# Performance work log

Hardware: AMD Instinct MI355X
Metric: run time of the kernel (lower is better)

The kernel has to match this reference:

```python
import jax, jax.numpy as jnp
import numpy as np

N_NODES = 100000
N_EDGES = 3200000
N_FEAT = 16
N_GRAPHS = 1024


def setup_inputs() -> dict:
    key = jax.random.key(0)
    ks = jax.random.split(key, 12)
    x = jax.random.normal(ks[0], (N_NODES, N_FEAT), dtype=jnp.float32)
    edge_index = jax.random.randint(ks[1], (2, N_EDGES), 0, N_NODES, dtype=jnp.int32)
    batch = jnp.sort(jax.random.randint(ks[2], (N_NODES,), 0, N_GRAPHS, dtype=jnp.int32))
    def lin(k, fan_in, fan_out):
        s = 1.0 / np.sqrt(fan_in)
        return jax.random.uniform(k, (fan_in, fan_out), jnp.float32, -s, s)
    W1 = lin(ks[3], N_FEAT, 64); b1 = jnp.zeros((64,), jnp.float32)
    W2 = lin(ks[4], 64, 32);     b2 = jnp.zeros((32,), jnp.float32)
    fc1_W = lin(ks[5], 32, 16);  fc1_b = jnp.zeros((16,), jnp.float32)
    fc2_W = lin(ks[6], 16, 1);   fc2_b = jnp.zeros((1,), jnp.float32)
    return {"x": x, "edge_index": edge_index, "batch": batch,
            "W1": W1, "b1": b1, "W2": W2, "b2": b2,
            "fc1_W": fc1_W, "fc1_b": fc1_b, "fc2_W": fc2_W, "fc2_b": fc2_b}


def _gcn_conv(h, W, b, src, dst, norm, n_nodes):
    # h: [N, Fin] -> [N, Fout]; symmetric-normalized scatter-add (PyG GCNConv)
    h = h @ W
    msg = h[src] * norm[:, None]            # edge-wise gather + scale
    out = jax.ops.segment_sum(msg, dst, num_segments=n_nodes)
    return out + b


def reference(x, edge_index, batch, W1, b1, W2, b2, fc1_W, fc1_b, fc2_W, fc2_b):
    n_nodes = x.shape[0]
    # add self-loops
    loops = jnp.arange(n_nodes, dtype=edge_index.dtype)
    src = jnp.concatenate([edge_index[0], loops])
    dst = jnp.concatenate([edge_index[1], loops])
    deg = jax.ops.segment_sum(jnp.ones_like(dst, dtype=x.dtype), dst, num_segments=n_nodes)
    dinv = jnp.where(deg > 0, jax.lax.rsqrt(deg), 0.0)
    norm = dinv[src] * dinv[dst]

    h = jax.nn.relu(_gcn_conv(x, W1, b1, src, dst, norm, n_nodes))
    # dropout p=0.2 is identity at inference
    h = jax.nn.relu(_gcn_conv(h, W2, b2, src, dst, norm, n_nodes))

    # global mean pool over graphs
    sums = jax.ops.segment_sum(h, batch, num_segments=N_GRAPHS)
    cnts = jax.ops.segment_sum(jnp.ones((n_nodes,), h.dtype), batch, num_segments=N_GRAPHS)
    g = sums / jnp.maximum(cnts, 1.0)[:, None]

    g = jax.nn.relu(g @ fc1_W + fc1_b)
    # dropout p=0.5 is identity at inference
    out = g @ fc2_W + fc2_b
    return jax.nn.sigmoid(out)  # [N_GRAPHS, 1]
```

## Files before the change

kernel.cpp:

```cpp
#include <hip/hip_runtime.h>
#include <math.h>

#define NNODES  100000
#define NEDGES  3200000
#define NGRAPHS 1024
#define BNODES  196
#define NBUCK   ((NNODES + BNODES - 1) / BNODES)
#define SCAP    12288
#define SLDS    7168
#define CHUNK   4096
#define NCHUNKS ((NEDGES + CHUNK - 1) / CHUNK)

typedef int iv4 __attribute__((ext_vector_type(4)));
typedef float fv2 __attribute__((ext_vector_type(2)));

#if defined(__has_builtin)
#if __has_builtin(__builtin_amdgcn_cvt_pk_f32_fp8) && __has_builtin(__builtin_amdgcn_cvt_pk_fp8_f32)
#define HW_FP8 1
#endif
#endif

__device__ __forceinline__ unsigned bf16pair(float a, float b) {
    unsigned ua = __float_as_uint(a), ub = __float_as_uint(b);
    ua += 0x7fffu + ((ua >> 16) & 1u);
    ub += 0x7fffu + ((ub >> 16) & 1u);
    return (ua >> 16) | (ub & 0xffff0000u);
}
__device__ __forceinline__ float bflo(unsigned u) { return __uint_as_float(u << 16); }
__device__ __forceinline__ float bfhi(unsigned u) { return __uint_as_float(u & 0xffff0000u); }

__device__ __forceinline__ unsigned fp8_of(float v) {
    unsigned s = (__float_as_uint(v) >> 24) & 0x80u;
    float a = fminf(fabsf(v), 448.f);
    unsigned ub = __float_as_uint(a);
    unsigned lsb = (ub >> 20) & 1u;
    ub += 0x0007FFFFu + lsb;
    int em = (int)(ub >> 20) - (120 << 3);
    if (em < 1) return s;
    if (em > 0x7E) em = 0x7E;
    return s | (unsigned)em;
}
__device__ __forceinline__ float fp8_to_f(unsigned b) {
    unsigned em = b & 0x7Fu;
    unsigned s = (b & 0x80u) << 24;
    float f = __uint_as_float(s | ((em + 0x3C0u) << 20));
    return (em >= 8u) ? f : 0.f;
}
__device__ __forceinline__ unsigned fp8x4_pack(float a, float b, float c, float d) {
    a = fminf(fmaxf(a, -448.f), 448.f);
    b = fminf(fmaxf(b, -448.f), 448.f);
    c = fminf(fmaxf(c, -448.f), 448.f);
    d = fminf(fmaxf(d, -448.f), 448.f);
#ifdef HW_FP8
    int w = __builtin_amdgcn_cvt_pk_fp8_f32(a, b, 0, false);
    w = __builtin_amdgcn_cvt_pk_fp8_f32(c, d, w, true);
    return (unsigned)w;
#else
    return fp8_of(a) | (fp8_of(b) << 8) | (fp8_of(c) << 16) | (fp8_of(d) << 24);
#endif
}
__device__ __forceinline__ fv2 f8lo(unsigned w) {
#ifdef HW_FP8
    return __builtin_amdgcn_cvt_pk_f32_fp8((int)w, false);
#else
    fv2 t; t.x = fp8_to_f(w & 0xFFu); t.y = fp8_to_f((w >> 8) & 0xFFu); return t;
#endif
}
__device__ __forceinline__ fv2 f8hi(unsigned w) {
#ifdef HW_FP8
    return __builtin_amdgcn_cvt_pk_f32_fp8((int)w, true);
#else
    fv2 t; t.x = fp8_to_f((w >> 16) & 0xFFu); t.y = fp8_to_f(w >> 24); return t;
#endif
}


__global__ void zero4_kernel(int4* p, int nvec) {
    int i = blockIdx.x * blockDim.x + threadIdx.x;
    if (i < nvec) p[i] = make_int4(0, 0, 0, 0);
}


__global__ void binA_kernel(const int* __restrict__ src, const int* __restrict__ dst,
                            int* __restrict__ bucketCur, int* __restrict__ stage) {
    __shared__ int lcnt[NBUCK + 1];
    __shared__ int boff[NBUCK + 1];
    __shared__ int gbase[NBUCK + 1];
    __shared__ int cur[NBUCK + 1];
    __shared__ int wtot[4];
    __shared__ int packed[CHUNK];
    __shared__ unsigned short bof[CHUNK];
    int tid = threadIdx.x;
    int beg = blockIdx.x * CHUNK;
    int end = beg + CHUNK; if (end > NEDGES) end = NEDGES;
    int cnt = end - beg;

    for (int i = tid; i <= NBUCK; i += 256) lcnt[i] = 0;
    __syncthreads();

    int ent[16];
    int bk[16];
#pragma unroll
    for (int it = 0; it < 4; ++it) {
        int e0 = beg + tid * 4 + it * 1024;
        if (e0 < end) {
            iv4 d4 = __builtin_nontemporal_load((const iv4*)(dst + e0));
            iv4 s4 = __builtin_nontemporal_load((const iv4*)(src + e0));
            int b;
            b = d4.x / BNODES; ent[it*4+0] = s4.x | ((d4.x - b*BNODES) << 17); bk[it*4+0] = b; atomicAdd(&lcnt[b], 1);
            b = d4.y / BNODES; ent[it*4+1] = s4.y | ((d4.y - b*BNODES) << 17); bk[it*4+1] = b; atomicAdd(&lcnt[b], 1);
            b = d4.z / BNODES; ent[it*4+2] = s4.z | ((d4.z - b*BNODES) << 17); bk[it*4+2] = b; atomicAdd(&lcnt[b], 1);
            b = d4.w / BNODES; ent[it*4+3] = s4.w | ((d4.w - b*BNODES) << 17); bk[it*4+3] = b; atomicAdd(&lcnt[b], 1);
        } else {
            bk[it*4+0] = -1; bk[it*4+1] = -1; bk[it*4+2] = -1; bk[it*4+3] = -1;
            ent[it*4+0] = 0; ent[it*4+1] = 0; ent[it*4+2] = 0; ent[it*4+3] = 0;
        }
    }
    __syncthreads();

    int b0 = 2 * tid, b1 = 2 * tid + 1;
    int c0 = lcnt[b0];
    int c1 = (b1 < NBUCK) ? lcnt[b1] : 0;
    int sum = c0 + c1;
    int lane = tid & 63, wid = tid >> 6;
    int v = sum;
#pragma unroll
    for (int o = 1; o < 64; o <<= 1) {
        int t = __shfl_up(v, o, 64);
        if (lane >= o) v += t;
    }
    if (lane == 63) wtot[wid] = v;
    __syncthreads();
    int woff = 0;
#pragma unroll
    for (int w = 0; w < 4; ++w) woff += (w < wid) ? wtot[w] : 0;
    int excl = woff + v - sum;
    boff[b0] = excl; cur[b0] = excl;
    if (b1 < NBUCK) { boff[b1] = excl + c0; cur[b1] = excl + c0; }
    if (c0 > 0) gbase[b0] = atomicAdd(&bucketCur[b0], c0);
    if (b1 < NBUCK && c1 > 0) gbase[b1] = atomicAdd(&bucketCur[b1], c1);
    __syncthreads();

#pragma unroll
    for (int k = 0; k < 16; ++k) {
        int b = bk[k];
        if (b >= 0) {
            int p = atomicAdd(&cur[b], 1);
            packed[p] = ent[k];
            bof[p] = (unsigned short)b;
        }
    }
    __syncthreads();

    for (int i = tid; i < cnt; i += 256) {
        int b = bof[i];
        int addr = b * SCAP + gbase[b] + (i - boff[b]);
        stage[addr] = packed[i];
    }
}


__global__ void scanE_kernel(const int* __restrict__ bucketCur, int* __restrict__ ebase) {
    int lane = threadIdx.x;
    int run = 0;
    for (int base = 0; base < NBUCK; base += 64) {
        int idx = base + lane;
        int own = (idx < NBUCK) ? bucketCur[idx] : 0;
        int v = own;
        for (int o = 1; o < 64; o <<= 1) {
            int t = __shfl_up(v, o, 64);
            if (lane >= o) v += t;
        }
        if (idx < NBUCK) ebase[idx] = run + v - own;
        run += __shfl(v, 63, 64);
    }
}


__global__ void binB_kernel(const int* __restrict__ bucketCur, const int* __restrict__ ebase,
                            const int* __restrict__ stage, const float2* __restrict__ x,
                            int* __restrict__ entries, int* __restrict__ rowptr,
                            float* __restrict__ dinv, unsigned* __restrict__ xs) {
    __shared__ int s[256];
    __shared__ int ncur[256];
    __shared__ float ndinv[256];
    __shared__ int wt[4];
    __shared__ int se[SLDS];
    int b = blockIdx.x;
    int cntE = bucketCur[b];
    int eb = ebase[b];
    int nlo = b * BNODES;
    int nn = NNODES - nlo; if (nn > BNODES) nn = BNODES;
    int sb = b * SCAP;
    int tid = threadIdx.x;

    s[tid] = 0;
    __syncthreads();
    for (int e = tid; e < cntE; e += 256) {
        int w = stage[sb + e];
        if (e < SLDS) se[e] = w;
        atomicAdd(&s[(unsigned)w >> 17], 1);
    }
    __syncthreads();
    int v = s[tid];
    int lane = tid & 63, wid = tid >> 6;
    int iv = v;
#pragma unroll
    for (int o = 1; o < 64; o <<= 1) {
        int t = __shfl_up(iv, o, 64);
        if (lane >= o) iv += t;
    }
    if (lane == 63) wt[wid] = iv;
    __syncthreads();
    int woff = 0;
#pragma unroll
    for (int w2 = 0; w2 < 4; ++w2) woff += (w2 < wid) ? wt[w2] : 0;
    int excl = woff + iv - v;
    ncur[tid] = excl;
    if (tid < nn) {
        rowptr[nlo + tid] = eb + excl;
        float di = rsqrtf((float)(v + 1));
        dinv[nlo + tid] = di;
        ndinv[tid] = di;
    }
    if (b == NBUCK - 1 && tid == 0) rowptr[NNODES] = NEDGES;
    __syncthreads();
    for (int i = tid; i < nn * 8; i += 256) {
        int node = i >> 3, w = i & 7;
        float2 v2 = x[(size_t)(nlo + node) * 8 + w];
        float di = ndinv[node];
        xs[(nlo + node) * 8 + w] = bf16pair(v2.x * di, v2.y * di);
    }
    for (int e = tid; e < cntE; e += 256) {
        unsigned w = (unsigned)((e < SLDS) ? se[e] : stage[sb + e]);
        int dl = (int)(w >> 17);
        int slot = atomicAdd(&ncur[dl], 1);
        entries[eb + slot] = (int)(w & 0x1FFFFu);
    }
}


__device__ __forceinline__ void acc_bf(unsigned u, fv2& a) {
    fv2 t; t.x = bflo(u); t.y = bfhi(u);
    a += t;
}
#define ACCX4(V) { acc_bf((V).x, acc0); acc_bf((V).y, acc1); acc_bf((V).z, acc2); acc_bf((V).w, acc3); }
#define QRED(a) { a.x += __shfl_xor(a.x, 2); a.y += __shfl_xor(a.y, 2); \
                  a.x += __shfl_xor(a.x, 4); a.y += __shfl_xor(a.y, 4); }

__global__ void __launch_bounds__(256) gatherX_kernel(const int* __restrict__ entries,
        const int* __restrict__ rowptr,
        const float* __restrict__ dinv, const uint4* __restrict__ xsv,
        float4* __restrict__ agg) {
    int t = blockIdx.x * 256 + threadIdx.x;
    int n = t >> 3, lane = t & 7;
    int half = lane & 1, quad = lane >> 1;
    int beg = rowptr[n], end = rowptr[n + 1];
    fv2 acc0 = {0.f, 0.f}, acc1 = {0.f, 0.f}, acc2 = {0.f, 0.f}, acc3 = {0.f, 0.f};
    if (quad == 0) {
        uint4 sv = xsv[n * 2 + half];
        ACCX4(sv);
    }

    int nb = (end - beg) >> 4;
    const int* ep = entries + beg + (quad << 2);
    iv4 e = {0, 0, 0, 0};
    if (nb > 0) __builtin_memcpy(&e, ep, 16);
    for (int i = 1; i <= nb; ++i) {
        iv4 f = e;
        if (i < nb) __builtin_memcpy(&e, ep + (i << 4), 16);
        uint4 v0 = xsv[f.x * 2 + half];
        uint4 v1 = xsv[f.y * 2 + half];
        uint4 v2 = xsv[f.z * 2 + half];
        uint4 v3 = xsv[f.w * 2 + half];
        ACCX4(v0); ACCX4(v1); ACCX4(v2); ACCX4(v3);
    }
    int tp = beg + (nb << 4) + (quad << 2);
#pragma unroll
    for (int j = 0; j < 4; ++j) {
        if (tp + j < end) {
            int ee = entries[tp + j];
            uint4 v = xsv[ee * 2 + half];
            ACCX4(v);
        }
    }

    QRED(acc0); QRED(acc1); QRED(acc2); QRED(acc3);

    if (quad == 0) {
        float di = dinv[n];
        float4 o0, o1;
        o0.x = acc0.x * di; o0.y = acc0.y * di; o0.z = acc1.x * di; o0.w = acc1.y * di;
        o1.x = acc2.x * di; o1.y = acc2.y * di; o1.z = acc3.x * di; o1.w = acc3.y * di;
        agg[n * 4 + half * 2 + 0] = o0;
        agg[n * 4 + half * 2 + 1] = o1;
    }
}


__global__ void __launch_bounds__(256) mlp_kernel(const float4* __restrict__ agg,
        const float* __restrict__ dinv,
        const float* __restrict__ W1, const float* __restrict__ b1,
        const float* __restrict__ W2, unsigned* __restrict__ hm2f) {
    __shared__ __align__(16) float w1s[16 * 64];
    __shared__ __align__(16) float w2s[64 * 32];
    __shared__ float bb1[64];
    __shared__ __align__(16) float h1s[32][68];
    int tid = threadIdx.x;
    for (int i = tid; i < 16 * 64; i += 256) w1s[i] = W1[i];
    for (int i = tid; i < 64 * 32; i += 256) w2s[i] = W2[i];
    if (tid < 64) bb1[tid] = b1[tid];

    int nl = tid >> 3, lane = tid & 7;
    int n = blockIdx.x * 32 + nl;
    const float4* ag = agg + n * 4;
    float4 A0 = ag[0], A1 = ag[1], A2 = ag[2], A3 = ag[3];
    float a[16] = {A0.x, A0.y, A0.z, A0.w, A1.x, A1.y, A1.z, A1.w,
                   A2.x, A2.y, A2.z, A2.w, A3.x, A3.y, A3.z, A3.w};
    __syncthreads();

    {
        int j0 = lane * 8;
        float h[8];
#pragma unroll
        for (int jj = 0; jj < 8; ++jj) h[jj] = bb1[j0 + jj];
#pragma unroll
        for (int k = 0; k < 16; ++k) {
            const float4* wr = (const float4*)(w1s + k * 64 + j0);
            float4 wa = wr[0], wb = wr[1];
            float av = a[k];
            h[0] += av * wa.x; h[1] += av * wa.y; h[2] += av * wa.z; h[3] += av * wa.w;
            h[4] += av * wb.x; h[5] += av * wb.y; h[6] += av * wb.z; h[7] += av * wb.w;
        }
        float4 r0, r1;
        r0.x = fmaxf(h[0], 0.f); r0.y = fmaxf(h[1], 0.f); r0.z = fmaxf(h[2], 0.f); r0.w = fmaxf(h[3], 0.f);
        r1.x = fmaxf(h[4], 0.f); r1.y = fmaxf(h[5], 0.f); r1.z = fmaxf(h[6], 0.f); r1.w = fmaxf(h[7], 0.f);
        float4* hw = (float4*)(&h1s[nl][j0]);
        hw[0] = r0; hw[1] = r1;
    }
    __syncthreads();

    {
        int j0 = lane * 4;
        float c0 = 0.f, c1 = 0.f, c2 = 0.f, c3 = 0.f;
#pragma unroll
        for (int k = 0; k < 64; k += 4) {
            float4 hv = *(const float4*)(&h1s[nl][k]);
            float4 w0 = *(const float4*)(w2s + (k + 0) * 32 + j0);
            float4 w1v = *(const float4*)(w2s + (k + 1) * 32 + j0);
            float4 w2v = *(const float4*)(w2s + (k + 2) * 32 + j0);
            float4 w3 = *(const float4*)(w2s + (k + 3) * 32 + j0);
            c0 += hv.x * w0.x; c1 += hv.x * w0.y; c2 += hv.x * w0.z; c3 += hv.x * w0.w;
            c0 += hv.y * w1v.x; c1 += hv.y * w1v.y; c2 += hv.y * w1v.z; c3 += hv.y * w1v.w;
            c0 += hv.z * w2v.x; c1 += hv.z * w2v.y; c2 += hv.z * w2v.z; c3 += hv.z * w2v.w;
            c0 += hv.w * w3.x; c1 += hv.w * w3.y; c2 += hv.w * w3.z; c3 += hv.w * w3.w;
        }
        float sc = dinv[n] * 64.f;
        hm2f[n * 8 + lane] = fp8x4_pack(c0 * sc, c1 * sc, c2 * sc, c3 * sc);
    }
}


#define ACCH4(V) { q0lo += f8lo((V).x); q0hi += f8hi((V).x); \
                   q1lo += f8lo((V).y); q1hi += f8hi((V).y); \
                   q2lo += f8lo((V).z); q2hi += f8hi((V).z); \
                   q3lo += f8lo((V).w); q3hi += f8hi((V).w); }

__global__ void __launch_bounds__(256) gatherH_pool_kernel(const int* __restrict__ entries,
        const int* __restrict__ rowptr,
        const float* __restrict__ dinv, const uint4* __restrict__ hm4,
        const float4* __restrict__ b2, const int* __restrict__ batch,
        float* __restrict__ psum, float* __restrict__ pcnt) {
    __shared__ float lps[8][32];
    __shared__ float lpc[8];
    int tid = threadIdx.x;
    ((float*)lps)[tid] = 0.f;
    if (tid < 8) lpc[tid] = 0.f;
    __syncthreads();

    int t = blockIdx.x * 256 + tid;
    int n = t >> 3, lane = t & 7;
    int half = lane & 1, quad = lane >> 1;
    int g0 = batch[blockIdx.x * 32];
    int beg = rowptr[n], end = rowptr[n + 1];
    fv2 q0lo = {0.f,0.f}, q0hi = {0.f,0.f}, q1lo = {0.f,0.f}, q1hi = {0.f,0.f},
        q2lo = {0.f,0.f}, q2hi = {0.f,0.f}, q3lo = {0.f,0.f}, q3hi = {0.f,0.f};
    if (quad == 0) {
        uint4 sv = hm4[n * 2 + half];
        ACCH4(sv);
    }

    int nb = (end - beg) >> 4;
    const int* ep = entries + beg + (quad << 2);
    iv4 e = {0, 0, 0, 0};
    if (nb > 0) __builtin_memcpy(&e, ep, 16);
    for (int i = 1; i <= nb; ++i) {
        iv4 f = e;
        if (i < nb) __builtin_memcpy(&e, ep + (i << 4), 16);
        uint4 v0 = hm4[f.x * 2 + half];
        uint4 v1 = hm4[f.y * 2 + half];
        uint4 v2 = hm4[f.z * 2 + half];
        uint4 v3 = hm4[f.w * 2 + half];
        ACCH4(v0); ACCH4(v1); ACCH4(v2); ACCH4(v3);
    }
    int tp = beg + (nb << 4) + (quad << 2);
#pragma unroll
    for (int j = 0; j < 4; ++j) {
        if (tp + j < end) {
            int ee = entries[tp + j];
            uint4 v = hm4[ee * 2 + half];
            ACCH4(v);
        }
    }

    QRED(q0lo); QRED(q0hi); QRED(q1lo); QRED(q1hi);
    QRED(q2lo); QRED(q2hi); QRED(q3lo); QRED(q3hi);

    if (quad == 0) {
        float sc = dinv[n] * (1.0f / 64.f);
        float4 bv0 = b2[half * 4 + 0], bv1 = b2[half * 4 + 1],
               bv2 = b2[half * 4 + 2], bv3 = b2[half * 4 + 3];
        float vv[16];
        vv[0]  = fmaxf(q0lo.x * sc + bv0.x, 0.f);
        vv[1]  = fmaxf(q0lo.y * sc + bv0.y, 0.f);
        vv[2]  = fmaxf(q0hi.x * sc + bv0.z, 0.f);
        vv[3]  = fmaxf(q0hi.y * sc + bv0.w, 0.f);
        vv[4]  = fmaxf(q1lo.x * sc + bv1.x, 0.f);
        vv[5]  = fmaxf(q1lo.y * sc + bv1.y, 0.f);
        vv[6]  = fmaxf(q1hi.x * sc + bv1.z, 0.f);
        vv[7]  = fmaxf(q1hi.y * sc + bv1.w, 0.f);
        vv[8]  = fmaxf(q2lo.x * sc + bv2.x, 0.f);
        vv[9]  = fmaxf(q2lo.y * sc + bv2.y, 0.f);
        vv[10] = fmaxf(q2hi.x * sc + bv2.z, 0.f);
        vv[11] = fmaxf(q2hi.y * sc + bv2.w, 0.f);
        vv[12] = fmaxf(q3lo.x * sc + bv3.x, 0.f);
        vv[13] = fmaxf(q3lo.y * sc + bv3.y, 0.f);
        vv[14] = fmaxf(q3hi.x * sc + bv3.z, 0.f);
        vv[15] = fmaxf(q3hi.y * sc + bv3.w, 0.f);

        int g = batch[n], gr = g - g0;
        if (gr < 8) {
            float* pg = &lps[gr][half * 16];
#pragma unroll
            for (int k2 = 0; k2 < 16; ++k2) atomicAdd(pg + k2, vv[k2]);
            if (lane == 0) atomicAdd(&lpc[gr], 1.0f);
        } else {
            float* pg = psum + g * 32 + half * 16;
#pragma unroll
            for (int k2 = 0; k2 < 16; ++k2) atomicAdd(pg + k2, vv[k2]);
            if (lane == 0) atomicAdd(&pcnt[g], 1.0f);
        }
    }
    __syncthreads();
    int grf = tid >> 5, f = tid & 31;
    float v = lps[grf][f];
    if (v != 0.f) atomicAdd(&psum[(g0 + grf) * 32 + f], v);
    if (f == 0) {
        float c = lpc[grf];
        if (c != 0.f) atomicAdd(&pcnt[g0 + grf], c);
    }
}


__global__ void head_kernel(const float* __restrict__ psum, const float* __restrict__ pcnt,
                            const float* __restrict__ fc1W, const float* __restrict__ fc1b,
                            const float* __restrict__ fc2W, const float* __restrict__ fc2b,
                            float* __restrict__ out) {
    int g = blockIdx.x * blockDim.x + threadIdx.x;
    if (g >= NGRAPHS) return;
    float inv = 1.0f / fmaxf(pcnt[g], 1.0f);
    float gv[32];
#pragma unroll
    for (int k = 0; k < 32; ++k) gv[k] = psum[g * 32 + k] * inv;
    float o = fc2b[0];
#pragma unroll
    for (int j = 0; j < 16; ++j) {
        float h = fc1b[j];
#pragma unroll
        for (int k = 0; k < 32; ++k) h += gv[k] * fc1W[k * 16 + j];
        h = fmaxf(h, 0.f);
        o += h * fc2W[j];
    }
    out[g] = 1.0f / (1.0f + expf(-o));
}


extern "C" void kernel_launch(void* const* d_in, const int* in_sizes, int n_in,
                              void* d_out, int out_size, void* d_ws, size_t ws_size,
                              hipStream_t stream) {
    const float* x    = (const float*)d_in[0];
    const int*   ei   = (const int*)d_in[1];
    const int*   batch= (const int*)d_in[2];
    const float* W1   = (const float*)d_in[3];
    const float* b1   = (const float*)d_in[4];
    const float* W2   = (const float*)d_in[5];
    const float* b2   = (const float*)d_in[6];
    const float* fc1W = (const float*)d_in[7];
    const float* fc1b = (const float*)d_in[8];
    const float* fc2W = (const float*)d_in[9];
    const float* fc2b = (const float*)d_in[10];
    float* out = (float*)d_out;

    const int* src = ei;
    const int* dst = ei + NEDGES;

    char* wsb = (char*)d_ws;
    int*      bucketCur = (int*)wsb;
    float*    psum      = (float*)(wsb + 2048);
    float*    pcnt      = (float*)(wsb + 133120);
    int*      ebase     = (int*)(wsb + 137216);
    float*    dinv      = (float*)(wsb + 139264);
    int*      rowptr    = (int*)(wsb + 539264);
    int*      stage     = (int*)(wsb + 939392);
    int*      entries   = (int*)(wsb + 26056064);
    unsigned* xs        = (unsigned*)(wsb + 38856064);
    unsigned* hm2f      = (unsigned*)(wsb + 42056064);
    float4*   agg       = (float4*)(wsb + 939392);

    const int B = 256;
    zero4_kernel<<<(8576 + B - 1) / B, B, 0, stream>>>((int4*)wsb, 8576);

    binA_kernel<<<NCHUNKS, B, 0, stream>>>(src, dst, bucketCur, stage);
    scanE_kernel<<<1, 64, 0, stream>>>(bucketCur, ebase);
    binB_kernel<<<NBUCK, B, 0, stream>>>(bucketCur, ebase, stage, (const float2*)x,
                                         entries, rowptr, dinv, xs);

    const int GTH = NNODES * 8 / B;
    gatherX_kernel<<<GTH, B, 0, stream>>>(entries, rowptr, dinv,
                                          (const uint4*)xs, agg);
    mlp_kernel<<<NNODES / 32, B, 0, stream>>>((const float4*)agg, dinv, W1, b1, W2, hm2f);
    gatherH_pool_kernel<<<GTH, B, 0, stream>>>(entries, rowptr, dinv,
                                               (const uint4*)hm2f, (const float4*)b2,
                                               batch, psum, pcnt);
    head_kernel<<<(NGRAPHS + B - 1) / B, B, 0, stream>>>(psum, pcnt, fc1W, fc1b, fc2W, fc2b, out);
}
```

Measured before the change: 241.8 us.

## Fuse layer-1 gather with dense MLP into one kernel using shuffles

Merges the layer-1 neighbor gather kernel and the per-node MLP kernel into a single kernel. The aggregated 16-float row is exchanged between the paired lanes with shuffles, and the 64-wide hidden vector is broadcast with width-8 shuffles. This replaces the agg round trip through global memory and the h1 round trip through shared memory. It also removes one launch. The cost is that every gather block now loads W1/W2 into LDS (about 12KB) and syncs before gathering, which may reduce occupancy.

```diff
diff --git a/kernel.cpp b/kernel.cpp
--- a/kernel.cpp
+++ b/kernel.cpp
@@ -248,11 +248,21 @@
 #define QRED(a) { a.x += __shfl_xor(a.x, 2); a.y += __shfl_xor(a.y, 2); \
                   a.x += __shfl_xor(a.x, 4); a.y += __shfl_xor(a.y, 4); }
 
-__global__ void __launch_bounds__(256) gatherX_kernel(const int* __restrict__ entries,
-        const int* __restrict__ rowptr,
-        const float* __restrict__ dinv, const uint4* __restrict__ xsv,
-        float4* __restrict__ agg) {
-    int t = blockIdx.x * 256 + threadIdx.x;
+__global__ void __launch_bounds__(256) gatherX_mlp_kernel(const int* __restrict__ entries,
+        const int* __restrict__ rowptr, const float* __restrict__ dinv,
+        const uint4* __restrict__ xsv,
+        const float* __restrict__ W1, const float* __restrict__ b1,
+        const float* __restrict__ W2, unsigned* __restrict__ hm2f) {
+    __shared__ __align__(16) float w1s[16 * 64];
+    __shared__ __align__(16) float w2s[64 * 32];
+    __shared__ float bb1[64];
+    int tid = threadIdx.x;
+    for (int i = tid; i < 16 * 64; i += 256) w1s[i] = W1[i];
+    for (int i = tid; i < 64 * 32; i += 256) w2s[i] = W2[i];
+    if (tid < 64) bb1[tid] = b1[tid];
+    __syncthreads();
+
+    int t = blockIdx.x * 256 + tid;
     int n = t >> 3, lane = t & 7;
     int half = lane & 1, quad = lane >> 1;
     int beg = rowptr[n], end = rowptr[n + 1];
@@ -287,75 +297,46 @@
 
     QRED(acc0); QRED(acc1); QRED(acc2); QRED(acc3);
 
-    if (quad == 0) {
-        float di = dinv[n];
-        float4 o0, o1;
-        o0.x = acc0.x * di; o0.y = acc0.y * di; o0.z = acc1.x * di; o0.w = acc1.y * di;
-        o1.x = acc2.x * di; o1.y = acc2.y * di; o1.z = acc3.x * di; o1.w = acc3.y * di;
-        agg[n * 4 + half * 2 + 0] = o0;
-        agg[n * 4 + half * 2 + 1] = o1;
-    }
-}
-
-
-__global__ void __launch_bounds__(256) mlp_kernel(const float4* __restrict__ agg,
-        const float* __restrict__ dinv,
-        const float* __restrict__ W1, const float* __restrict__ b1,
-        const float* __restrict__ W2, unsigned* __restrict__ hm2f) {
-    __shared__ __align__(16) float w1s[16 * 64];
-    __shared__ __align__(16) float w2s[64 * 32];
-    __shared__ float bb1[64];
-    __shared__ __align__(16) float h1s[32][68];
-    int tid = threadIdx.x;
-    for (int i = tid; i < 16 * 64; i += 256) w1s[i] = W1[i];
-    for (int i = tid; i < 64 * 32; i += 256) w2s[i] = W2[i];
-    if (tid < 64) bb1[tid] = b1[tid];
-
-    int nl = tid >> 3, lane = tid & 7;
-    int n = blockIdx.x * 32 + nl;
-    const float4* ag = agg + n * 4;
-    float4 A0 = ag[0], A1 = ag[1], A2 = ag[2], A3 = ag[3];
-    float a[16] = {A0.x, A0.y, A0.z, A0.w, A1.x, A1.y, A1.z, A1.w,
-                   A2.x, A2.y, A2.z, A2.w, A3.x, A3.y, A3.z, A3.w};
-    __syncthreads();
-
+    float di = dinv[n];
+    float own[8];
+    own[0] = acc0.x * di; own[1] = acc0.y * di; own[2] = acc1.x * di; own[3] = acc1.y * di;
+    own[4] = acc2.x * di; own[5] = acc2.y * di; own[6] = acc3.x * di; own[7] = acc3.y * di;
+    float oth[8];
+#pragma unroll
+    for (int i2 = 0; i2 < 8; ++i2) oth[i2] = __shfl_xor(own[i2], 1);
+    float a16[16];
+#pragma unroll
+    for (int k = 0; k < 8; ++k) a16[k]     = (half == 0) ? own[k] : oth[k];
+#pragma unroll
+    for (int k = 0; k < 8; ++k) a16[8 + k] = (half == 0) ? oth[k] : own[k];
+
+    float h[8];
     {
         int j0 = lane * 8;
-        float h[8];
 #pragma unroll
         for (int jj = 0; jj < 8; ++jj) h[jj] = bb1[j0 + jj];
 #pragma unroll
         for (int k = 0; k < 16; ++k) {
             const float4* wr = (const float4*)(w1s + k * 64 + j0);
             float4 wa = wr[0], wb = wr[1];
-            float av = a[k];
+            float av = a16[k];
             h[0] += av * wa.x; h[1] += av * wa.y; h[2] += av * wa.z; h[3] += av * wa.w;
             h[4] += av * wb.x; h[5] += av * wb.y; h[6] += av * wb.z; h[7] += av * wb.w;
         }
-        float4 r0, r1;
-        r0.x = fmaxf(h[0], 0.f); r0.y = fmaxf(h[1], 0.f); r0.z = fmaxf(h[2], 0.f); r0.w = fmaxf(h[3], 0.f);
-        r1.x = fmaxf(h[4], 0.f); r1.y = fmaxf(h[5], 0.f); r1.z = fmaxf(h[6], 0.f); r1.w = fmaxf(h[7], 0.f);
-        float4* hw = (float4*)(&h1s[nl][j0]);
-        hw[0] = r0; hw[1] = r1;
-    }
-    __syncthreads();
+#pragma unroll
+        for (int jj = 0; jj < 8; ++jj) h[jj] = fmaxf(h[jj], 0.f);
+    }
 
     {
-        int j0 = lane * 4;
+        int j0c = lane * 4;
         float c0 = 0.f, c1 = 0.f, c2 = 0.f, c3 = 0.f;
 #pragma unroll
-        for (int k = 0; k < 64; k += 4) {
-            float4 hv = *(const float4*)(&h1s[nl][k]);
-            float4 w0 = *(const float4*)(w2s + (k + 0) * 32 + j0);
-            float4 w1v = *(const float4*)(w2s + (k + 1) * 32 + j0);
-            float4 w2v = *(const float4*)(w2s + (k + 2) * 32 + j0);
-            float4 w3 = *(const float4*)(w2s + (k + 3) * 32 + j0);
-            c0 += hv.x * w0.x; c1 += hv.x * w0.y; c2 += hv.x * w0.z; c3 += hv.x * w0.w;
-            c0 += hv.y * w1v.x; c1 += hv.y * w1v.y; c2 += hv.y * w1v.z; c3 += hv.y * w1v.w;
-            c0 += hv.z * w2v.x; c1 += hv.z * w2v.y; c2 += hv.z * w2v.z; c3 += hv.z * w2v.w;
-            c0 += hv.w * w3.x; c1 += hv.w * w3.y; c2 += hv.w * w3.z; c3 += hv.w * w3.w;
-        }
-        float sc = dinv[n] * 64.f;
+        for (int k = 0; k < 64; ++k) {
+            float hv = __shfl(h[k & 7], k >> 3, 8);
+            float4 w = *(const float4*)(w2s + k * 32 + j0c);
+            c0 += hv * w.x; c1 += hv * w.y; c2 += hv * w.z; c3 += hv * w.w;
+        }
+        float sc = di * 64.f;
         hm2f[n * 8 + lane] = fp8x4_pack(c0 * sc, c1 * sc, c2 * sc, c3 * sc);
     }
 }
@@ -515,7 +496,6 @@
     int*      entries   = (int*)(wsb + 26056064);
     unsigned* xs        = (unsigned*)(wsb + 38856064);
     unsigned* hm2f      = (unsigned*)(wsb + 42056064);
-    float4*   agg       = (float4*)(wsb + 939392);
 
     const int B = 256;
     zero4_kernel<<<(8576 + B - 1) / B, B, 0, stream>>>((int4*)wsb, 8576);
@@ -526,9 +506,8 @@
                                          entries, rowptr, dinv, xs);
 
     const int GTH = NNODES * 8 / B;
-    gatherX_kernel<<<GTH, B, 0, stream>>>(entries, rowptr, dinv,
-                                          (const uint4*)xs, agg);
-    mlp_kernel<<<NNODES / 32, B, 0, stream>>>((const float4*)agg, dinv, W1, b1, W2, hm2f);
+    gatherX_mlp_kernel<<<GTH, B, 0, stream>>>(entries, rowptr, dinv,
+                                              (const uint4*)xs, W1, b1, W2, hm2f);
     gatherH_pool_kernel<<<GTH, B, 0, stream>>>(entries, rowptr, dinv,
                                                (const uint4*)hm2f, (const float4*)b2,
                                                batch, psum, pcnt);
```

After: 239.9 us. Within noise of the previous version (-0.8%).
